# Kernel tuning notes

Measured on AMD Instinct MI355X. Metric: run time of the kernel, lower is better.

The kernel has to match this reference:

```python
import jax, jax.numpy as jnp
import numpy as np

B, S, N, F, H = 8, 12, 4096, 4, 64  # batch, seq_len, num_nodes, input_dim, hidden_dim


def setup_inputs() -> dict:
    key = jax.random.key(0)
    ks = jax.random.split(key, 16)
    sc = 0.05
    adj = jax.random.uniform(ks[0], (N, N), jnp.float32) * (2.0 / N)  # ~row-normalized Laplacian
    return {
        "X": jax.random.normal(ks[1], (B, S, N, F), jnp.float32),
        "adj": adj,
        "struc_emb": jax.random.normal(ks[2], (N, H), jnp.float32),
        "W1": jax.random.normal(ks[3], (H + F, 3 * H), jnp.float32) * sc,
        "b1": jnp.ones((3 * H,), jnp.float32),  # bias=1.0 init in graph_conv1
        "W2": jax.random.normal(ks[4], (H + F, H), jnp.float32) * sc,
        "b2": jnp.zeros((H,), jnp.float32),
        "W_ih": jax.random.normal(ks[5], (4 * H, H), jnp.float32) * sc,
        "W_hh": jax.random.normal(ks[6], (4 * H, H), jnp.float32) * sc,
        "b_ih": jnp.zeros((4 * H,), jnp.float32),
        "b_hh": jnp.zeros((4 * H,), jnp.float32),
        "D1": jax.random.normal(ks[7], (H, H // 2), jnp.float32) * sc,
        "bd1": jnp.zeros((H // 2,), jnp.float32),
        "D2": jax.random.normal(ks[8], (H // 2, 1), jnp.float32) * sc,
        "bd2": jnp.zeros((1,), jnp.float32),
    }


def _graph_conv(adj, x_t, h_flat, W, b, out_dim):
    # x_t: [B,N,F]; h_flat: [B, N*H]
    h = h_flat.reshape(B, N, H)
    cat = jnp.concatenate([x_t, h], axis=-1)            # [B,N,F+H]
    a = jnp.einsum('mn,bnf->bmf', adj, cat)             # laplacian diffusion
    out = a @ W + b                                     # [B,N,out_dim]
    return out.reshape(B, N * out_dim)


def reference(X, adj, struc_emb, W1, b1, W2, b2, W_ih, W_hh, b_ih, b_hh, D1, bd1, D2, bd2):
    # ---- encoder: TGTCCellLSTM unrolled over time (cell_state never updated, as in source) ----
    h0 = jnp.broadcast_to(struc_emb.reshape(1, N * H), (B, N * H))
    c0 = h0  # cell returns old cell_state, so it stays the struc_emb forever (faithful)

    def enc_step(h, x_t):
        g = jax.nn.sigmoid(_graph_conv(adj, x_t, h, W1, b1, 3 * H))   # [B, N*3H]
        f, i, o = jnp.split(g, 3, axis=1)                             # flat chunk, as in torch code
        conv = _graph_conv(adj, x_t, h, W2, b2, H)                    # [B, N*H]
        c = f * c0 + i * jnp.tanh(conv)
        h_new = o * jnp.tanh(c)
        return h_new, None

    h_last, _ = jax.lax.scan(enc_step, h0, jnp.swapaxes(X, 0, 1))  # scan over S
    z = h_last.reshape(B, N, H)

    # ---- decoder: 1-layer LSTM fed the same z at every step, then 2-layer MLP to scalar ----
    x_dec = z.reshape(B * N, H)
    x_gates = x_dec @ W_ih.T + b_ih + b_hh  # input contribution constant across steps

    def dec_step(carry, _):
        h, c = carry
        gates = x_gates + h @ W_hh.T
        i, f, g, o = jnp.split(gates, 4, axis=1)  # torch LSTM gate order
        c = jax.nn.sigmoid(f) * c + jax.nn.sigmoid(i) * jnp.tanh(g)
        h = jax.nn.sigmoid(o) * jnp.tanh(c)
        return (h, c), h

    zeros = jnp.zeros((B * N, H), X.dtype)
    _, hs = jax.lax.scan(dec_step, (zeros, zeros), None, length=S)  # [S, B*N, H]
    hs = jnp.swapaxes(hs, 0, 1)                                      # [B*N, S, H]
    d = jax.nn.relu(hs @ D1 + bd1) @ D2 + bd2                        # [B*N, S, 1]
    recon = d.reshape(B, S, N)  # flat reshape from (B*N, S), matching torch reshape semantics
    return (z, recon)
```

## Files before the change

### kernel.cpp

```cpp
#include <hip/hip_runtime.h>
#include <cstdint>
#include <cstddef>


typedef unsigned short u16;
typedef short s8v __attribute__((ext_vector_type(8)));
typedef unsigned short h8v __attribute__((ext_vector_type(8)));
typedef float f4v __attribute__((ext_vector_type(4)));
typedef int   i4v __attribute__((ext_vector_type(4)));

__device__ __forceinline__ u16 f2bf(float x){
  union { float f; uint32_t u; } v; v.f = x;
  uint32_t r = v.u + 0x7FFFu + ((v.u >> 16) & 1u);
  return (u16)(r >> 16);
}
__device__ __forceinline__ float bf2f(u16 x){
  union { uint32_t u; float f; } v; v.u = ((uint32_t)x) << 16; return v.f;
}
__device__ __forceinline__ float frcp(float x){ return __builtin_amdgcn_rcpf(x); }
__device__ __forceinline__ float fsig(float x){ return frcp(1.0f + __expf(-x)); }
__device__ __forceinline__ float ftanh(float x){ return 1.0f - 2.0f * frcp(1.0f + __expf(2.0f * x)); }
__device__ __forceinline__ int8_t f2i8(float x){
  int v = (int)rintf(x);
  v = v > 127 ? 127 : (v < -127 ? -127 : v);
  return (int8_t)v;
}

typedef const __attribute__((address_space(1))) unsigned int* gp_t;
typedef __attribute__((address_space(3))) unsigned int* lp_t;
__device__ __forceinline__ void glds16(const void* g, void* l){
  __builtin_amdgcn_global_load_lds((gp_t)g, (lp_t)l, 16, 0, 0);
}

__global__ __launch_bounds__(256)
void gemm_s1_i8(const int8_t* __restrict__ A, const int8_t* __restrict__ Bt,
                u16* __restrict__ Cpart, int Ncols, int ksl, float cscale)
{
  __shared__ int8_t As[2 * 128 * 128];
  __shared__ int8_t Bs[2 * 128 * 128];
  const int t  = threadIdx.x;
  const int l  = t & 63;
  const int w  = t >> 6;
  const int wm = (w >> 1) * 64;
  const int wc = (w & 1) * 64;
  const int mb = blockIdx.x * 128;
  const int nb = blockIdx.y * 128;
  const int k0 = blockIdx.z * ksl;

  i4v acc[4][4];
  #pragma unroll
  for (int i = 0; i < 4; ++i)
    #pragma unroll
    for (int j = 0; j < 4; ++j) acc[i][j] = (i4v)0;

  const int srow = t >> 3;
  const int gsw  = ((t & 7) ^ (srow & 7)) * 16;
  const int8_t* ab = A  + (size_t)(mb + srow) * 4096 + k0 + gsw;
  const int8_t* bb = Bt + (size_t)(nb + srow) * 4096 + k0 + gsw;

  const int rA = l & 15;
  const int lsw = l & 7;

  #pragma unroll
  for (int j = 0; j < 4; ++j) {
    glds16(ab + (size_t)(32 * j) * 4096, As + j * 4096 + t * 16);
    glds16(bb + (size_t)(32 * j) * 4096, Bs + j * 4096 + t * 16);
  }

  for (int kk = 0; kk < ksl; kk += 128) {
    const int cur = (kk >> 7) & 1;
    __syncthreads();
    if (kk + 128 < ksl) {
      const int nxt = cur ^ 1;
      #pragma unroll
      for (int j = 0; j < 4; ++j) {
        glds16(ab + (size_t)(32 * j) * 4096 + kk + 128, As + nxt * 16384 + j * 4096 + t * 16);
        glds16(bb + (size_t)(32 * j) * 4096 + kk + 128, Bs + nxt * 16384 + j * 4096 + t * 16);
      }
    }
    const int bofs = cur * 16384;
    #pragma unroll
    for (int sub = 0; sub < 2; ++sub) {
      const int kpos = ((sub * 4 + (l >> 4)) ^ lsw) * 16;
      i4v af[4], bf[4];
      #pragma unroll
      for (int mt = 0; mt < 4; ++mt)
        af[mt] = *(const i4v*)&As[bofs + (wm + mt * 16 + rA) * 128 + kpos];
      #pragma unroll
      for (int nt = 0; nt < 4; ++nt)
        bf[nt] = *(const i4v*)&Bs[bofs + (wc + nt * 16 + rA) * 128 + kpos];
      #pragma unroll
      for (int mt = 0; mt < 4; ++mt)
        #pragma unroll
        for (int nt = 0; nt < 4; ++nt)
          acc[mt][nt] = __builtin_amdgcn_mfma_i32_16x16x64_i8(af[mt], bf[nt], acc[mt][nt], 0, 0, 0);
    }
  }

  u16* Cs = Cpart + (size_t)blockIdx.z * 4096 * Ncols;
  const int colo = l & 15;
  const int rowo = (l >> 4) * 4;
  #pragma unroll
  for (int mt = 0; mt < 4; ++mt)
    #pragma unroll
    for (int nt = 0; nt < 4; ++nt)
      #pragma unroll
      for (int r = 0; r < 4; ++r) {
        int gr = mb + wm + mt * 16 + rowo + r;
        int gc = nb + wc + nt * 16 + colo;
        Cs[(size_t)gr * Ncols + gc] = f2bf((float)acc[mt][nt][r] * cscale);
      }
}

__global__ __launch_bounds__(256)
void reduceN(const u16* __restrict__ P, u16* __restrict__ O, size_t SL)
{
  size_t i = ((size_t)blockIdx.x * 256 + threadIdx.x) * 8;
  if (i >= SL) return;
  float s[8] = {0,0,0,0,0,0,0,0};
  #pragma unroll
  for (int z = 0; z < 4; ++z) {
    uint4 v = *(const uint4*)(P + z * SL + i);
    uint32_t wd[4] = {v.x, v.y, v.z, v.w};
    #pragma unroll
    for (int q = 0; q < 4; ++q) {
      union { uint32_t u; float f; } lo, hi;
      lo.u = wd[q] << 16; hi.u = wd[q] & 0xFFFF0000u;
      s[2*q] += lo.f; s[2*q+1] += hi.f;
    }
  }
  uint4 o; uint32_t* ow = (uint32_t*)&o;
  #pragma unroll
  for (int q = 0; q < 4; ++q)
    ow[q] = (uint32_t)f2bf(s[2*q]) | ((uint32_t)f2bf(s[2*q+1]) << 16);
  *(uint4*)(O + i) = o;
}

__global__ __launch_bounds__(256)
void gemm_s2(const u16* __restrict__ AH, const u16* __restrict__ AXb,
             const u16* __restrict__ WTf, const float* __restrict__ b1v,
             const float* __restrict__ b2v, u16* __restrict__ G, int tstep)
{
  __shared__ u16 As[64 * 104];
  const int t = threadIdx.x;
  const int l = t & 63, w = t >> 6;
  const int wm = (w >> 1) * 32, wc0 = (w & 1) * 32;
  const int mb = blockIdx.x * 64;
  const size_t SL = 32768ull * 64;

  #pragma unroll
  for (int pass = 0; pass < 2; ++pass) {
    int idx = t + pass * 256;
    int row = idx >> 3, oct = idx & 7;
    size_t base = (size_t)(mb + row) * 64 + oct * 8;
    float s[8] = {0,0,0,0,0,0,0,0};
    #pragma unroll
    for (int z = 0; z < 4; ++z) {
      uint4 v = *(const uint4*)(AH + z * SL + base);
      uint32_t wd[4] = {v.x, v.y, v.z, v.w};
      #pragma unroll
      for (int q = 0; q < 4; ++q) {
        union { uint32_t u; float f; } lo, hi;
        lo.u = wd[q] << 16; hi.u = wd[q] & 0xFFFF0000u;
        s[2*q] += lo.f; s[2*q+1] += hi.f;
      }
    }
    uint4 o; uint32_t* ow = (uint32_t*)&o;
    #pragma unroll
    for (int q = 0; q < 4; ++q)
      ow[q] = (uint32_t)f2bf(s[2*q]) | ((uint32_t)f2bf(s[2*q+1]) << 16);
    *(uint4*)&As[row * 104 + oct * 8] = o;
  }
  {
    int row = t >> 2, q = t & 3;
    uint4 o = {0, 0, 0, 0};
    if (q == 0) {
      int r = mb + row, n = r >> 3, b = r & 7;
      const uint32_t* src = (const uint32_t*)(AXb + (size_t)n * 384 + tstep * 32 + b * 4);
      o.x = src[0]; o.y = src[1];
    }
    *(uint4*)&As[row * 104 + 64 + q * 8] = o;
  }
  __syncthreads();

  const int rA = l & 15, kg = (l >> 4) * 8;
  s8v af[3][2];
  #pragma unroll
  for (int kc = 0; kc < 3; ++kc)
    #pragma unroll
    for (int mt = 0; mt < 2; ++mt)
      af[kc][mt] = *(const s8v*)&As[(wm + mt * 16 + rA) * 104 + kc * 32 + kg];

  const int lchunk = ((l & 15) * 4 + (l >> 4)) * 8;
  const int colo = l & 15, rowo = (l >> 4) * 4;
  #pragma unroll
  for (int nb4 = 0; nb4 < 4; ++nb4) {
    const int wc = nb4 * 64 + wc0;
    f4v acc[2][2];
    #pragma unroll
    for (int i = 0; i < 2; ++i)
      #pragma unroll
      for (int j = 0; j < 2; ++j) acc[i][j] = (f4v)0.0f;
    #pragma unroll
    for (int kc = 0; kc < 3; ++kc) {
      s8v bf[2];
      #pragma unroll
      for (int nt = 0; nt < 2; ++nt) {
        int ct = nb4 * 4 + (w & 1) * 2 + nt;
        bf[nt] = *(const s8v*)&WTf[(ct * 3 + kc) * 512 + lchunk];
      }
      #pragma unroll
      for (int mt = 0; mt < 2; ++mt)
        #pragma unroll
        for (int nt = 0; nt < 2; ++nt)
          acc[mt][nt] = __builtin_amdgcn_mfma_f32_16x16x32_bf16(af[kc][mt], bf[nt], acc[mt][nt], 0, 0, 0);
    }
    #pragma unroll
    for (int mt = 0; mt < 2; ++mt)
      #pragma unroll
      for (int nt = 0; nt < 2; ++nt) {
        int gc = wc + nt * 16 + colo;
        float bb = (gc < 192) ? b1v[gc] : b2v[gc - 192];
        #pragma unroll
        for (int r = 0; r < 4; ++r) {
          int gr = mb + wm + mt * 16 + rowo + r;
          int np = gr >> 3, b = gr & 7;
          float v = acc[mt][nt][r] + bb;
          size_t addr;
          u16 val;
          if (gc < 192) {
            int p = np * 192 + gc;
            int role = p >> 18;
            int k = p & 262143;
            addr = ((size_t)(role * 8 + b) << 18) + k;
            val = f2bf(fsig(v));
          } else {
            int k = np * 64 + (gc - 192);
            addr = ((size_t)(24 + b) << 18) + k;
            val = f2bf(ftanh(v));
          }
          G[addr] = val;
        }
      }
  }
}

__global__ __launch_bounds__(256)
void enc_update(const u16* __restrict__ G, const float* __restrict__ struc,
                int8_t* __restrict__ PB, float* __restrict__ zout,
                u16* __restrict__ zbf, int last)
{
  __shared__ uint8_t hx[64 * 40];
  const int t = threadIdx.x;
  const int b = blockIdx.x >> 7;
  const int n0 = (blockIdx.x & 127) * 32;
  const int k8 = n0 * 64 + t * 8;
  const int nloc = t >> 3;
  const int hh0 = (t & 7) * 8;

  h8v f8 = *(const h8v*)&G[((size_t)(     b) << 18) + k8];
  h8v i8_ = *(const h8v*)&G[((size_t)( 8 + b) << 18) + k8];
  h8v o8 = *(const h8v*)&G[((size_t)(16 + b) << 18) + k8];
  h8v c8 = *(const h8v*)&G[((size_t)(24 + b) << 18) + k8];
  float4 s0 = *(const float4*)&struc[k8];
  float4 s1 = *(const float4*)&struc[k8 + 4];
  float sv[8] = {s0.x, s0.y, s0.z, s0.w, s1.x, s1.y, s1.z, s1.w};

  float hv[8];
  #pragma unroll
  for (int j = 0; j < 8; ++j) {
    float c = bf2f(f8[j]) * sv[j] + bf2f(i8_[j]) * bf2f(c8[j]);
    hv[j] = bf2f(o8[j]) * ftanh(c);
    hx[(hh0 + j) * 40 + nloc] = (uint8_t)f2i8(hv[j] * 127.0f);
  }
  if (last) {
    float4 z0 = {hv[0], hv[1], hv[2], hv[3]};
    float4 z1 = {hv[4], hv[5], hv[6], hv[7]};
    *(float4*)&zout[((size_t)b << 18) + k8] = z0;
    *(float4*)&zout[((size_t)b << 18) + k8 + 4] = z1;
    h8v zb;
    #pragma unroll
    for (int j = 0; j < 8; ++j) zb[j] = f2bf(hv[j]);
    *(h8v*)&zbf[((size_t)b << 18) + k8] = zb;
  }
  __syncthreads();
  {
    int row = t >> 2, seg = t & 3;
    uint2 v = *(const uint2*)&hx[row * 40 + seg * 8];
    *(uint2*)&PB[(size_t)(b * 64 + row) * 4096 + n0 + seg * 8] = v;
  }
}

__global__ __launch_bounds__(256)
void setup_all(const float* __restrict__ adj, int8_t* __restrict__ adj_i8,
               const float* __restrict__ W1, const float* __restrict__ W2,
               const float* __restrict__ Wih, const float* __restrict__ Whh,
               const float* __restrict__ D1,
               u16* __restrict__ WTf, u16* __restrict__ WihB,
               u16* __restrict__ WhhB, u16* __restrict__ D1t,
               const float* __restrict__ struc, int8_t* __restrict__ PB,
               const float* __restrict__ X, int8_t* __restrict__ Xp)
{
  const int blk = blockIdx.x;
  const int t = threadIdx.x;
  if (blk < 16384) {
    size_t i = ((size_t)blk * 256 + t) * 4;
    float4 v = *(const float4*)(adj + i);
    const float s = 127.0f * 2048.0f;
    char4 o;
    o.x = f2i8(v.x * s); o.y = f2i8(v.y * s); o.z = f2i8(v.z * s); o.w = f2i8(v.w * s);
    *(char4*)(adj_i8 + i) = o;
  } else if (blk < 16616) {
    int gid = (blk - 16384) * 256 + t;
    if (gid < 24576) {
      int f = gid >> 9;
      int q = gid & 511;
      int ct = f / 3, kc = f - ct * 3;
      int c = q >> 3, e = q & 7;
      int rA = c >> 2, g = c & 3;
      int row = ct * 16 + rA;
      int ch = kc * 32 + g * 8 + e;
      float v = 0.0f;
      int rr = (ch < 64) ? (ch + 4) : (ch < 68 ? ch - 64 : -1);
      if (rr >= 0) v = (row < 192) ? W1[(size_t)rr * 192 + row] : W2[(size_t)rr * 64 + (row - 192)];
      WTf[gid] = f2bf(v);
    } else if (gid < 40960) {
      int q = gid - 24576; WihB[q] = f2bf(Wih[q]);
    } else if (gid < 57344) {
      int q = gid - 40960; WhhB[q] = f2bf(Whh[q]);
    } else if (gid < 59392) {
      int q = gid - 57344;
      int j = q >> 6, hh = q & 63;
      D1t[q] = f2bf(D1[(size_t)hh * 32 + j]);
    }
  } else if (blk < 24808) {
    int gid = (blk - 16616) * 256 + t;
    int n = gid & 4095;
    int r = gid >> 12;
    int hh = r & 63;
    PB[(size_t)r * 4096 + n] = f2i8(struc[(size_t)n * 64 + hh] * 25.4f);
  } else {
    int gid = (blk - 24808) * 256 + t;
    int n = gid & 4095;
    int col = gid >> 12;
    int ts = col >> 5, r = col & 31, b = r >> 2, f = r & 3;
    Xp[(size_t)col * 4096 + n] = f2i8(X[(((size_t)(b * 12 + ts)) * 4096 + n) * 4 + f] * 25.4f);
  }
}

#define DSTR 80
__global__ __launch_bounds__(512, 4)
void dec_fused(const u16* __restrict__ zbf, const u16* __restrict__ WihB,
               const u16* __restrict__ WhhB,
               const float* __restrict__ bih, const float* __restrict__ bhh,
               const u16* __restrict__ D1t, const float* __restrict__ bd1,
               const float* __restrict__ D2, const float* __restrict__ bd2,
               float* __restrict__ recon)
{
  __shared__ u16 whl[256 * DSTR];
  __shared__ u16 hl[64 * DSTR];
  const int t = threadIdx.x;
  const int l = t & 63;
  const int w = t >> 6;
  const int wg = w >> 1;
  const int half = w & 1;
  const int r0 = blockIdx.x * 64;
  const int rA = l & 15;
  const int kg = (l >> 4) * 8;

  for (int c = t; c < 2048; c += 512) {
    int j = c >> 3, k8 = (c & 7) * 8;
    *(uint4*)&whl[j * DSTR + k8] = *(const uint4*)&WhhB[j * 64 + k8];
  }

  f4v xg[8];
  {
    s8v a0 = *(const s8v*)&zbf[(size_t)(r0 + wg * 16 + rA) * 64 + kg];
    s8v a1 = *(const s8v*)&zbf[(size_t)(r0 + wg * 16 + rA) * 64 + 32 + kg];
    #pragma unroll
    for (int j = 0; j < 8; ++j) {
      int nt = (j >> 1) * 4 + half * 2 + (j & 1);
      s8v b0 = *(const s8v*)&WihB[(nt * 16 + rA) * 64 + kg];
      s8v b1 = *(const s8v*)&WihB[(nt * 16 + rA) * 64 + 32 + kg];
      f4v a = (f4v)0.0f;
      a = __builtin_amdgcn_mfma_f32_16x16x32_bf16(a0, b0, a, 0, 0, 0);
      a = __builtin_amdgcn_mfma_f32_16x16x32_bf16(a1, b1, a, 0, 0, 0);
      float bb = bih[nt * 16 + rA] + bhh[nt * 16 + rA];
      #pragma unroll
      for (int r = 0; r < 4; ++r) xg[j][r] = a[r] + bb;
    }
  }
  s8v d1f[4];
  #pragma unroll
  for (int nt2 = 0; nt2 < 2; ++nt2)
    #pragma unroll
    for (int kc = 0; kc < 2; ++kc)
      d1f[nt2 * 2 + kc] = *(const s8v*)&D1t[(nt2 * 16 + rA) * 64 + kc * 32 + kg];
  const float bd1x = bd1[rA], bd1y = bd1[16 + rA];
  const float d2x = D2[rA], d2y = D2[16 + rA];
  const float bd2v = bd2[0];

  float cst[8];
  #pragma unroll
  for (int q = 0; q < 8; ++q) cst[q] = 0.0f;
  s8v ha0 = (s8v)0, ha1 = (s8v)0;
  __syncthreads();

  for (int s = 0; s < 12; ++s) {
    f4v acc[8];
    #pragma unroll
    for (int j = 0; j < 8; ++j) acc[j] = xg[j];
    if (s > 0) {
      #pragma unroll
      for (int j = 0; j < 8; ++j) {
        int nt = (j >> 1) * 4 + half * 2 + (j & 1);
        s8v b0 = *(const s8v*)&whl[(nt * 16 + rA) * DSTR + kg];
        s8v b1 = *(const s8v*)&whl[(nt * 16 + rA) * DSTR + 32 + kg];
        acc[j] = __builtin_amdgcn_mfma_f32_16x16x32_bf16(ha0, b0, acc[j], 0, 0, 0);
        acc[j] = __builtin_amdgcn_mfma_f32_16x16x32_bf16(ha1, b1, acc[j], 0, 0, 0);
      }
    }
    __syncthreads();
    #pragma unroll
    for (int ql = 0; ql < 2; ++ql) {
      int q = half * 2 + ql;
      #pragma unroll
      for (int r = 0; r < 4; ++r) {
        float i_ = fsig (acc[0 + ql][r]);
        float f_ = fsig (acc[2 + ql][r]);
        float g_ = ftanh(acc[4 + ql][r]);
        float o_ = fsig (acc[6 + ql][r]);
        float cc = f_ * cst[ql * 4 + r] + i_ * g_;
        cst[ql * 4 + r] = cc;
        float hv = o_ * ftanh(cc);
        hl[(wg * 16 + (l >> 4) * 4 + r) * DSTR + q * 16 + rA] = f2bf(hv);
      }
    }
    __syncthreads();
    ha0 = *(const s8v*)&hl[(wg * 16 + rA) * DSTR + kg];
    ha1 = *(const s8v*)&hl[(wg * 16 + rA) * DSTR + 32 + kg];
    if (half == 0) {
      f4v m0 = (f4v)0.0f, m1 = (f4v)0.0f;
      m0 = __builtin_amdgcn_mfma_f32_16x16x32_bf16(ha0, d1f[0], m0, 0, 0, 0);
      m0 = __builtin_amdgcn_mfma_f32_16x16x32_bf16(ha1, d1f[1], m0, 0, 0, 0);
      m1 = __builtin_amdgcn_mfma_f32_16x16x32_bf16(ha0, d1f[2], m1, 0, 0, 0);
      m1 = __builtin_amdgcn_mfma_f32_16x16x32_bf16(ha1, d1f[3], m1, 0, 0, 0);
      f4v p;
      #pragma unroll
      for (int r = 0; r < 4; ++r)
        p[r] = fmaxf(m0[r] + bd1x, 0.0f) * d2x + fmaxf(m1[r] + bd1y, 0.0f) * d2y;
      #pragma unroll
      for (int mask = 1; mask < 16; mask <<= 1)
        #pragma unroll
        for (int r = 0; r < 4; ++r) p[r] += __shfl_xor(p[r], mask);
      if (rA < 4)
        recon[(size_t)(r0 + wg * 16 + (l >> 4) * 4 + rA) * 12 + s] = p[rA] + bd2v;
    }
  }
}

extern "C" void kernel_launch(void* const* d_in, const int* in_sizes, int n_in,
                              void* d_out, int out_size, void* d_ws, size_t ws_size,
                              hipStream_t stream)
{
  (void)in_sizes; (void)n_in; (void)out_size; (void)ws_size;
  const float* X     = (const float*)d_in[0];
  const float* adj   = (const float*)d_in[1];
  const float* struc = (const float*)d_in[2];
  const float* W1    = (const float*)d_in[3];
  const float* b1    = (const float*)d_in[4];
  const float* W2    = (const float*)d_in[5];
  const float* b2    = (const float*)d_in[6];
  const float* Wih   = (const float*)d_in[7];
  const float* Whh   = (const float*)d_in[8];
  const float* bih   = (const float*)d_in[9];
  const float* bhh   = (const float*)d_in[10];
  const float* D1    = (const float*)d_in[11];
  const float* bd1   = (const float*)d_in[12];
  const float* D2    = (const float*)d_in[13];
  const float* bd2   = (const float*)d_in[14];

  char* ws = (char*)d_ws;
  size_t off = 0;
  auto alloc = [&](size_t bytes){ void* p = ws + off; off += (bytes + 255) & ~(size_t)255; return p; };
  int8_t* adj_i8 = (int8_t*)alloc(4096ull * 4096);
  int8_t* PB     = (int8_t*)alloc(512ull * 4096);
  int8_t* Xp     = (int8_t*)alloc(384ull * 4096);
  u16*   AXb    = (u16*)  alloc(4096ull * 384 * 2);
  u16*   Cpart  = (u16*)  alloc(4ull * 4096 * 512 * 2);
  u16*   G      = (u16*)  alloc(4ull * 8 * 262144 * 2);
  u16*   zbf    = (u16*)  alloc(32768ull * 64 * 2);
  u16*   WTf    = (u16*)  alloc(256ull * 96 * 2);
  u16*   WihB   = (u16*)  alloc(256ull * 64 * 2);
  u16*   WhhB   = (u16*)  alloc(256ull * 64 * 2);
  u16*   D1t    = (u16*)  alloc(32ull * 64 * 2);

  float* zout  = (float*)d_out;
  float* recon = (float*)d_out + 2097152;

  const float cs5 = (float)(2.0 / 4096.0 * 5.0 / (127.0 * 127.0));
  const float cs1 = (float)(2.0 / 4096.0 * 1.0 / (127.0 * 127.0));

  setup_all<<<30952, 256, 0, stream>>>(adj, adj_i8, W1, W2, Wih, Whh, D1,
                                       WTf, WihB, WhhB, D1t, struc, PB, X, Xp);
  gemm_s1_i8 <<<dim3(32, 3, 4), 256, 0, stream>>>(adj_i8, Xp, Cpart, 384, 1024, cs5);
  reduceN    <<<  768, 256, 0, stream>>>(Cpart, AXb, 4096ull * 384);

  for (int t = 0; t < 12; ++t) {
    gemm_s1_i8<<<dim3(32, 4, 4), 256, 0, stream>>>(adj_i8, PB, Cpart, 512, 1024,
                                                   t == 0 ? cs5 : cs1);
    gemm_s2<<<512, 256, 0, stream>>>(Cpart, AXb, WTf, b1, b2, G, t);
    enc_update<<<1024, 256, 0, stream>>>(G, struc, PB, zout, zbf, t == 11);
  }

  dec_fused<<<512, 512, 0, stream>>>(zbf, WihB, WhhB, bih, bhh,
                                     D1t, bd1, D2, bd2, recon);
}
```

Measured before the change: 556.9 us.

## Retile int8 adjacency GEMM to 512 threads with K=64 stages and merge first launch

The int8 adjacency GEMM core now runs with 512 threads in 8 waves, each covering 64x32 of the 128x128 tile. K stages are 64 wide, which halves shared memory and changes the swizzle. The step-0 hidden-state GEMM is merged with the X-projection GEMM into one combined launch of 7 column-block groups, with a separate partial buffer for the X side. This is meant to raise occupancy and latency hiding and to remove one launch. In exchange there are more K iterations and barriers per tile, and each wave gets less operand reuse.

```diff
diff --git a/kernel.cpp b/kernel.cpp
--- a/kernel.cpp
+++ b/kernel.cpp
@@ -32,84 +32,98 @@
   __builtin_amdgcn_global_load_lds((gp_t)g, (lp_t)l, 16, 0, 0);
 }
 
-__global__ __launch_bounds__(256)
-void gemm_s1_i8(const int8_t* __restrict__ A, const int8_t* __restrict__ Bt,
-                u16* __restrict__ Cpart, int Ncols, int ksl, float cscale)
-{
-  __shared__ int8_t As[2 * 128 * 128];
-  __shared__ int8_t Bs[2 * 128 * 128];
+__device__ __forceinline__ void s1_core(int8_t* As, int8_t* Bs,
+    const int8_t* __restrict__ A, const int8_t* __restrict__ Bt,
+    u16* __restrict__ Cs, int Ncols, int ksl, float cscale,
+    int mb, int nb, int k0)
+{
   const int t  = threadIdx.x;
   const int l  = t & 63;
   const int w  = t >> 6;
-  const int wm = (w >> 1) * 64;
-  const int wc = (w & 1) * 64;
-  const int mb = blockIdx.x * 128;
-  const int nb = blockIdx.y * 128;
-  const int k0 = blockIdx.z * ksl;
-
-  i4v acc[4][4];
+  const int wm = (w >> 2) * 64;
+  const int wc = (w & 3) * 32;
+  const int rA = l & 15;
+  const int kg4 = l >> 4;
+
+  i4v acc[4][2];
   #pragma unroll
   for (int i = 0; i < 4; ++i)
     #pragma unroll
-    for (int j = 0; j < 4; ++j) acc[i][j] = (i4v)0;
-
-  const int srow = t >> 3;
-  const int gsw  = ((t & 7) ^ (srow & 7)) * 16;
-  const int8_t* ab = A  + (size_t)(mb + srow) * 4096 + k0 + gsw;
-  const int8_t* bb = Bt + (size_t)(nb + srow) * 4096 + k0 + gsw;
-
-  const int rA = l & 15;
-  const int lsw = l & 7;
-
-  #pragma unroll
-  for (int j = 0; j < 4; ++j) {
-    glds16(ab + (size_t)(32 * j) * 4096, As + j * 4096 + t * 16);
-    glds16(bb + (size_t)(32 * j) * 4096, Bs + j * 4096 + t * 16);
-  }
-
-  for (int kk = 0; kk < ksl; kk += 128) {
-    const int cur = (kk >> 7) & 1;
+    for (int j = 0; j < 2; ++j) acc[i][j] = (i4v)0;
+
+  const int srow = t >> 2;
+  const int gofs = (((t & 3) + (srow >> 1)) & 3) * 16;
+  const int8_t* ab = A  + (size_t)(mb + srow) * 4096 + k0 + gofs;
+  const int8_t* bb = Bt + (size_t)(nb + srow) * 4096 + k0 + gofs;
+
+  glds16(ab, As + t * 16);
+  glds16(bb, Bs + t * 16);
+
+  const int kpos = ((kg4 - (rA >> 1)) & 3) * 16;
+
+  for (int kk = 0; kk < ksl; kk += 64) {
+    const int cur = (kk >> 6) & 1;
     __syncthreads();
-    if (kk + 128 < ksl) {
+    if (kk + 64 < ksl) {
       const int nxt = cur ^ 1;
-      #pragma unroll
-      for (int j = 0; j < 4; ++j) {
-        glds16(ab + (size_t)(32 * j) * 4096 + kk + 128, As + nxt * 16384 + j * 4096 + t * 16);
-        glds16(bb + (size_t)(32 * j) * 4096 + kk + 128, Bs + nxt * 16384 + j * 4096 + t * 16);
-      }
-    }
-    const int bofs = cur * 16384;
-    #pragma unroll
-    for (int sub = 0; sub < 2; ++sub) {
-      const int kpos = ((sub * 4 + (l >> 4)) ^ lsw) * 16;
-      i4v af[4], bf[4];
-      #pragma unroll
-      for (int mt = 0; mt < 4; ++mt)
-        af[mt] = *(const i4v*)&As[bofs + (wm + mt * 16 + rA) * 128 + kpos];
-      #pragma unroll
-      for (int nt = 0; nt < 4; ++nt)
-        bf[nt] = *(const i4v*)&Bs[bofs + (wc + nt * 16 + rA) * 128 + kpos];
-      #pragma unroll
-      for (int mt = 0; mt < 4; ++mt)
-        #pragma unroll
-        for (int nt = 0; nt < 4; ++nt)
-          acc[mt][nt] = __builtin_amdgcn_mfma_i32_16x16x64_i8(af[mt], bf[nt], acc[mt][nt], 0, 0, 0);
-    }
-  }
-
-  u16* Cs = Cpart + (size_t)blockIdx.z * 4096 * Ncols;
+      glds16(ab + kk + 64, As + nxt * 8192 + t * 16);
+      glds16(bb + kk + 64, Bs + nxt * 8192 + t * 16);
+    }
+    const int bofs = cur * 8192;
+    i4v af[4], bf[2];
+    #pragma unroll
+    for (int mt = 0; mt < 4; ++mt)
+      af[mt] = *(const i4v*)&As[bofs + (wm + mt * 16 + rA) * 64 + kpos];
+    #pragma unroll
+    for (int nt = 0; nt < 2; ++nt)
+      bf[nt] = *(const i4v*)&Bs[bofs + (wc + nt * 16 + rA) * 64 + kpos];
+    #pragma unroll
+    for (int mt = 0; mt < 4; ++mt)
+      #pragma unroll
+      for (int nt = 0; nt < 2; ++nt)
+        acc[mt][nt] = __builtin_amdgcn_mfma_i32_16x16x64_i8(af[mt], bf[nt], acc[mt][nt], 0, 0, 0);
+  }
+
   const int colo = l & 15;
   const int rowo = (l >> 4) * 4;
   #pragma unroll
   for (int mt = 0; mt < 4; ++mt)
     #pragma unroll
-    for (int nt = 0; nt < 4; ++nt)
+    for (int nt = 0; nt < 2; ++nt)
       #pragma unroll
       for (int r = 0; r < 4; ++r) {
         int gr = mb + wm + mt * 16 + rowo + r;
         int gc = nb + wc + nt * 16 + colo;
         Cs[(size_t)gr * Ncols + gc] = f2bf((float)acc[mt][nt][r] * cscale);
       }
+}
+
+__global__ __launch_bounds__(512, 4)
+void gemm_s1_i8(const int8_t* __restrict__ A, const int8_t* __restrict__ Bt,
+                u16* __restrict__ Cpart, int Ncols, int ksl, float cscale)
+{
+  __shared__ int8_t As[2 * 128 * 64];
+  __shared__ int8_t Bs[2 * 128 * 64];
+  s1_core(As, Bs, A, Bt, Cpart + (size_t)blockIdx.z * 4096 * Ncols,
+          Ncols, ksl, cscale, blockIdx.x * 128, blockIdx.y * 128,
+          blockIdx.z * ksl);
+}
+
+__global__ __launch_bounds__(512, 4)
+void gemm_s1_comb(const int8_t* __restrict__ A, const int8_t* __restrict__ Xp,
+                  const int8_t* __restrict__ PB,
+                  u16* __restrict__ CpX, u16* __restrict__ CpH,
+                  int ksl, float csX, float csH)
+{
+  __shared__ int8_t As[2 * 128 * 64];
+  __shared__ int8_t Bs[2 * 128 * 64];
+  const int by = blockIdx.y;
+  if (by < 3)
+    s1_core(As, Bs, A, Xp, CpX + (size_t)blockIdx.z * 4096 * 384,
+            384, ksl, csX, blockIdx.x * 128, by * 128, blockIdx.z * ksl);
+  else
+    s1_core(As, Bs, A, PB, CpH + (size_t)blockIdx.z * 4096 * 512,
+            512, ksl, csH, blockIdx.x * 128, (by - 3) * 128, blockIdx.z * ksl);
 }
 
 __global__ __launch_bounds__(256)
@@ -488,6 +502,7 @@
   int8_t* Xp     = (int8_t*)alloc(384ull * 4096);
   u16*   AXb    = (u16*)  alloc(4096ull * 384 * 2);
   u16*   Cpart  = (u16*)  alloc(4ull * 4096 * 512 * 2);
+  u16*   CpartX = (u16*)  alloc(4ull * 4096 * 384 * 2);
   u16*   G      = (u16*)  alloc(4ull * 8 * 262144 * 2);
   u16*   zbf    = (u16*)  alloc(32768ull * 64 * 2);
   u16*   WTf    = (u16*)  alloc(256ull * 96 * 2);
@@ -503,12 +518,13 @@
 
   setup_all<<<30952, 256, 0, stream>>>(adj, adj_i8, W1, W2, Wih, Whh, D1,
                                        WTf, WihB, WhhB, D1t, struc, PB, X, Xp);
-  gemm_s1_i8 <<<dim3(32, 3, 4), 256, 0, stream>>>(adj_i8, Xp, Cpart, 384, 1024, cs5);
-  reduceN    <<<  768, 256, 0, stream>>>(Cpart, AXb, 4096ull * 384);
+  gemm_s1_comb<<<dim3(32, 7, 4), 512, 0, stream>>>(adj_i8, Xp, PB, CpartX, Cpart,
+                                                   1024, cs5, cs5);
+  reduceN<<<768, 256, 0, stream>>>(CpartX, AXb, 4096ull * 384);
 
   for (int t = 0; t < 12; ++t) {
-    gemm_s1_i8<<<dim3(32, 4, 4), 256, 0, stream>>>(adj_i8, PB, Cpart, 512, 1024,
-                                                   t == 0 ? cs5 : cs1);
+    if (t > 0)
+      gemm_s1_i8<<<dim3(32, 4, 4), 512, 0, stream>>>(adj_i8, PB, Cpart, 512, 1024, cs1);
     gemm_s2<<<512, 256, 0, stream>>>(Cpart, AXb, WTf, b1, b2, G, t);
     enc_update<<<1024, 256, 0, stream>>>(G, struc, PB, zout, zbf, t == 11);
   }
```

New measurement: 586.7 us. 5.4% more time.

## Merge first adjacency GEMMs and fold final encoder update into decoder

Applied to the files above, without the earlier changes.

The adjacency×X GEMM and the first adjacency×h GEMM now run as one launch of 7 column-tile groups, which removes a launch and fills more CUs in that step. The final enc_update is dropped and its work (writing z and the bf16 copy for the decoder) moves into dec_fused, which computes z straight from the gate buffer into shared memory. This removes two kernel launches and the global round trip through the zbf buffer. The cost is a separate partial buffer for the X GEMM and extra setup work at the start of the decoder.

```diff
diff --git a/kernel.cpp b/kernel.cpp
--- a/kernel.cpp
+++ b/kernel.cpp
@@ -32,20 +32,16 @@
   __builtin_amdgcn_global_load_lds((gp_t)g, (lp_t)l, 16, 0, 0);
 }
 
-__global__ __launch_bounds__(256)
-void gemm_s1_i8(const int8_t* __restrict__ A, const int8_t* __restrict__ Bt,
-                u16* __restrict__ Cpart, int Ncols, int ksl, float cscale)
-{
-  __shared__ int8_t As[2 * 128 * 128];
-  __shared__ int8_t Bs[2 * 128 * 128];
+__device__ __forceinline__ void s1_core(int8_t* As, int8_t* Bs,
+    const int8_t* __restrict__ A, const int8_t* __restrict__ Bt,
+    u16* __restrict__ Cs, int Ncols, int ksl, float cscale,
+    int mb, int nb, int k0)
+{
   const int t  = threadIdx.x;
   const int l  = t & 63;
   const int w  = t >> 6;
   const int wm = (w >> 1) * 64;
   const int wc = (w & 1) * 64;
-  const int mb = blockIdx.x * 128;
-  const int nb = blockIdx.y * 128;
-  const int k0 = blockIdx.z * ksl;
 
   i4v acc[4][4];
   #pragma unroll
@@ -97,7 +93,6 @@
     }
   }
 
-  u16* Cs = Cpart + (size_t)blockIdx.z * 4096 * Ncols;
   const int colo = l & 15;
   const int rowo = (l >> 4) * 4;
   #pragma unroll
@@ -110,6 +105,34 @@
         int gc = nb + wc + nt * 16 + colo;
         Cs[(size_t)gr * Ncols + gc] = f2bf((float)acc[mt][nt][r] * cscale);
       }
+}
+
+__global__ __launch_bounds__(256)
+void gemm_s1_i8(const int8_t* __restrict__ A, const int8_t* __restrict__ Bt,
+                u16* __restrict__ Cpart, int Ncols, int ksl, float cscale)
+{
+  __shared__ int8_t As[2 * 128 * 128];
+  __shared__ int8_t Bs[2 * 128 * 128];
+  s1_core(As, Bs, A, Bt, Cpart + (size_t)blockIdx.z * 4096 * Ncols,
+          Ncols, ksl, cscale, blockIdx.x * 128, blockIdx.y * 128,
+          blockIdx.z * ksl);
+}
+
+__global__ __launch_bounds__(256)
+void gemm_s1_comb(const int8_t* __restrict__ A, const int8_t* __restrict__ Xp,
+                  const int8_t* __restrict__ PB,
+                  u16* __restrict__ CpX, u16* __restrict__ CpH,
+                  int ksl, float cs)
+{
+  __shared__ int8_t As[2 * 128 * 128];
+  __shared__ int8_t Bs[2 * 128 * 128];
+  const int by = blockIdx.y;
+  if (by < 3)
+    s1_core(As, Bs, A, Xp, CpX + (size_t)blockIdx.z * 4096 * 384,
+            384, ksl, cs, blockIdx.x * 128, by * 128, blockIdx.z * ksl);
+  else
+    s1_core(As, Bs, A, PB, CpH + (size_t)blockIdx.z * 4096 * 512,
+            512, ksl, cs, blockIdx.x * 128, (by - 3) * 128, blockIdx.z * ksl);
 }
 
 __global__ __launch_bounds__(256)
@@ -247,8 +270,7 @@
 
 __global__ __launch_bounds__(256)
 void enc_update(const u16* __restrict__ G, const float* __restrict__ struc,
-                int8_t* __restrict__ PB, float* __restrict__ zout,
-                u16* __restrict__ zbf, int last)
+                int8_t* __restrict__ PB)
 {
   __shared__ uint8_t hx[64 * 40];
   const int t = threadIdx.x;
@@ -266,22 +288,11 @@
   float4 s1 = *(const float4*)&struc[k8 + 4];
   float sv[8] = {s0.x, s0.y, s0.z, s0.w, s1.x, s1.y, s1.z, s1.w};
 
-  float hv[8];
   #pragma unroll
   for (int j = 0; j < 8; ++j) {
     float c = bf2f(f8[j]) * sv[j] + bf2f(i8_[j]) * bf2f(c8[j]);
-    hv[j] = bf2f(o8[j]) * ftanh(c);
-    hx[(hh0 + j) * 40 + nloc] = (uint8_t)f2i8(hv[j] * 127.0f);
-  }
-  if (last) {
-    float4 z0 = {hv[0], hv[1], hv[2], hv[3]};
-    float4 z1 = {hv[4], hv[5], hv[6], hv[7]};
-    *(float4*)&zout[((size_t)b << 18) + k8] = z0;
-    *(float4*)&zout[((size_t)b << 18) + k8 + 4] = z1;
-    h8v zb;
-    #pragma unroll
-    for (int j = 0; j < 8; ++j) zb[j] = f2bf(hv[j]);
-    *(h8v*)&zbf[((size_t)b << 18) + k8] = zb;
+    float hv = bf2f(o8[j]) * ftanh(c);
+    hx[(hh0 + j) * 40 + nloc] = (uint8_t)f2i8(hv * 127.0f);
   }
   __syncthreads();
   {
@@ -350,8 +361,9 @@
 
 #define DSTR 80
 __global__ __launch_bounds__(512, 4)
-void dec_fused(const u16* __restrict__ zbf, const u16* __restrict__ WihB,
-               const u16* __restrict__ WhhB,
+void dec_fused(const u16* __restrict__ G, const float* __restrict__ struc,
+               float* __restrict__ zout,
+               const u16* __restrict__ WihB, const u16* __restrict__ WhhB,
                const float* __restrict__ bih, const float* __restrict__ bhh,
                const u16* __restrict__ D1t, const float* __restrict__ bd1,
                const float* __restrict__ D2, const float* __restrict__ bd2,
@@ -359,6 +371,7 @@
 {
   __shared__ u16 whl[256 * DSTR];
   __shared__ u16 hl[64 * DSTR];
+  __shared__ u16 zl[64 * DSTR];
   const int t = threadIdx.x;
   const int l = t & 63;
   const int w = t >> 6;
@@ -373,10 +386,37 @@
     *(uint4*)&whl[j * DSTR + k8] = *(const uint4*)&WhhB[j * 64 + k8];
   }
 
+  {
+    const int b = r0 >> 12;
+    const size_t base = (size_t)(r0 & 4095) * 64 + t * 8;
+    h8v f8 = *(const h8v*)&G[((size_t)(     b) << 18) + base];
+    h8v i8_ = *(const h8v*)&G[((size_t)( 8 + b) << 18) + base];
+    h8v o8 = *(const h8v*)&G[((size_t)(16 + b) << 18) + base];
+    h8v c8 = *(const h8v*)&G[((size_t)(24 + b) << 18) + base];
+    float4 s0 = *(const float4*)&struc[base];
+    float4 s1 = *(const float4*)&struc[base + 4];
+    float sv[8] = {s0.x, s0.y, s0.z, s0.w, s1.x, s1.y, s1.z, s1.w};
+    float hv[8];
+    #pragma unroll
+    for (int j = 0; j < 8; ++j) {
+      float c = bf2f(f8[j]) * sv[j] + bf2f(i8_[j]) * bf2f(c8[j]);
+      hv[j] = bf2f(o8[j]) * ftanh(c);
+    }
+    float4 z0 = {hv[0], hv[1], hv[2], hv[3]};
+    float4 z1 = {hv[4], hv[5], hv[6], hv[7]};
+    *(float4*)&zout[((size_t)b << 18) + base] = z0;
+    *(float4*)&zout[((size_t)b << 18) + base + 4] = z1;
+    h8v zb;
+    #pragma unroll
+    for (int j = 0; j < 8; ++j) zb[j] = f2bf(hv[j]);
+    *(h8v*)&zl[(t >> 3) * DSTR + (t & 7) * 8] = zb;
+  }
+  __syncthreads();
+
   f4v xg[8];
   {
-    s8v a0 = *(const s8v*)&zbf[(size_t)(r0 + wg * 16 + rA) * 64 + kg];
-    s8v a1 = *(const s8v*)&zbf[(size_t)(r0 + wg * 16 + rA) * 64 + 32 + kg];
+    s8v a0 = *(const s8v*)&zl[(wg * 16 + rA) * DSTR + kg];
+    s8v a1 = *(const s8v*)&zl[(wg * 16 + rA) * DSTR + 32 + kg];
     #pragma unroll
     for (int j = 0; j < 8; ++j) {
       int nt = (j >> 1) * 4 + half * 2 + (j & 1);
@@ -404,7 +444,6 @@
   #pragma unroll
   for (int q = 0; q < 8; ++q) cst[q] = 0.0f;
   s8v ha0 = (s8v)0, ha1 = (s8v)0;
-  __syncthreads();
 
   for (int s = 0; s < 12; ++s) {
     f4v acc[8];
@@ -488,8 +527,8 @@
   int8_t* Xp     = (int8_t*)alloc(384ull * 4096);
   u16*   AXb    = (u16*)  alloc(4096ull * 384 * 2);
   u16*   Cpart  = (u16*)  alloc(4ull * 4096 * 512 * 2);
+  u16*   CpartX = (u16*)  alloc(4ull * 4096 * 384 * 2);
   u16*   G      = (u16*)  alloc(4ull * 8 * 262144 * 2);
-  u16*   zbf    = (u16*)  alloc(32768ull * 64 * 2);
   u16*   WTf    = (u16*)  alloc(256ull * 96 * 2);
   u16*   WihB   = (u16*)  alloc(256ull * 64 * 2);
   u16*   WhhB   = (u16*)  alloc(256ull * 64 * 2);
@@ -503,16 +542,18 @@
 
   setup_all<<<30952, 256, 0, stream>>>(adj, adj_i8, W1, W2, Wih, Whh, D1,
                                        WTf, WihB, WhhB, D1t, struc, PB, X, Xp);
-  gemm_s1_i8 <<<dim3(32, 3, 4), 256, 0, stream>>>(adj_i8, Xp, Cpart, 384, 1024, cs5);
-  reduceN    <<<  768, 256, 0, stream>>>(Cpart, AXb, 4096ull * 384);
+  gemm_s1_comb<<<dim3(32, 7, 4), 256, 0, stream>>>(adj_i8, Xp, PB, CpartX, Cpart,
+                                                   1024, cs5);
+  reduceN<<<768, 256, 0, stream>>>(CpartX, AXb, 4096ull * 384);
 
   for (int t = 0; t < 12; ++t) {
-    gemm_s1_i8<<<dim3(32, 4, 4), 256, 0, stream>>>(adj_i8, PB, Cpart, 512, 1024,
-                                                   t == 0 ? cs5 : cs1);
+    if (t > 0)
+      gemm_s1_i8<<<dim3(32, 4, 4), 256, 0, stream>>>(adj_i8, PB, Cpart, 512, 1024, cs1);
     gemm_s2<<<512, 256, 0, stream>>>(Cpart, AXb, WTf, b1, b2, G, t);
-    enc_update<<<1024, 256, 0, stream>>>(G, struc, PB, zout, zbf, t == 11);
-  }
-
-  dec_fused<<<512, 512, 0, stream>>>(zbf, WihB, WhhB, bih, bhh,
+    if (t < 11)
+      enc_update<<<1024, 256, 0, stream>>>(G, struc, PB);
+  }
+
+  dec_fused<<<512, 512, 0, stream>>>(G, struc, zout, WihB, WhhB, bih, bhh,
                                      D1t, bd1, D2, bd2, recon);
 }
```

After: 549.1 us. About the same (-1.4%).
